# Kernel optimization log

Measured on AMD Instinct MI355X. Metric: run time of the kernel, lower is better.

The kernel has to match this reference:

```python
import jax, jax.numpy as jnp
import numpy as np

B, S, D, H, HD, FF, L = 16384, 5, 6, 2, 3, 2048, 4
EPS = 1e-5


def setup_inputs() -> dict:
    key = jax.random.key(0)
    ks = jax.random.split(key, 20)
    s = lambda fan: 1.0 / np.sqrt(fan)
    inp = {
        'x': jax.random.normal(ks[0], (B, S, D), dtype=jnp.float32),
        # per-layer stacked MHA params (in_proj split into q/k/v) and out_proj
        'Wq': jax.random.uniform(ks[1], (L, D, D), jnp.float32, -s(D), s(D)),
        'bq': jax.random.uniform(ks[2], (L, D), jnp.float32, -s(D), s(D)),
        'Wk': jax.random.uniform(ks[3], (L, D, D), jnp.float32, -s(D), s(D)),
        'bk': jax.random.uniform(ks[4], (L, D), jnp.float32, -s(D), s(D)),
        'Wv': jax.random.uniform(ks[5], (L, D, D), jnp.float32, -s(D), s(D)),
        'bv': jax.random.uniform(ks[6], (L, D), jnp.float32, -s(D), s(D)),
        'Wo': jax.random.uniform(ks[7], (L, D, D), jnp.float32, -s(D), s(D)),
        'bo': jax.random.uniform(ks[8], (L, D), jnp.float32, -s(D), s(D)),
        # FFN: linear1 D->FF, linear2 FF->D (torch Linear stores [out,in])
        'W1': jax.random.uniform(ks[9], (L, FF, D), jnp.float32, -s(D), s(D)),
        'b1': jax.random.uniform(ks[10], (L, FF), jnp.float32, -s(D), s(D)),
        'W2': jax.random.uniform(ks[11], (L, D, FF), jnp.float32, -s(FF), s(FF)),
        'b2': jax.random.uniform(ks[12], (L, D), jnp.float32, -s(FF), s(FF)),
        # layernorms
        'g1': jnp.ones((L, D), jnp.float32),
        'be1': jnp.zeros((L, D), jnp.float32),
        'g2': jnp.ones((L, D), jnp.float32),
        'be2': jnp.zeros((L, D), jnp.float32),
        # classification head Linear(30, 2)
        'Wfc': jax.random.uniform(ks[13], (2, S * D), jnp.float32, -s(S * D), s(S * D)),
        'bfc': jax.random.uniform(ks[14], (2,), jnp.float32, -s(S * D), s(S * D)),
    }
    return inp


def _layernorm(x, g, b):
    m = jnp.mean(x, axis=-1, keepdims=True)
    v = jnp.mean(jnp.square(x - m), axis=-1, keepdims=True)
    return (x - m) * jax.lax.rsqrt(v + EPS) * g + b


def _encoder_stack(x, Wq, bq, Wk, bk, Wv, bv, Wo, bo, W1, b1, W2, b2, g1, be1, g2, be2):
    scale = 1.0 / np.sqrt(HD)
    for i in range(L):  # small fixed loop over layers
        # multi-head self-attention (post-norm, eval mode: dropout = identity)
        q = (x @ Wq[i].T + bq[i]).reshape(B, S, H, HD)
        k = (x @ Wk[i].T + bk[i]).reshape(B, S, H, HD)
        v = (x @ Wv[i].T + bv[i]).reshape(B, S, H, HD)
        scores = jnp.einsum('bqhd,bkhd->bhqk', q, k) * scale
        attn = jax.nn.softmax(scores, axis=-1)
        ctx = jnp.einsum('bhqk,bkhd->bqhd', attn, v).reshape(B, S, D)
        x = _layernorm(x + ctx @ Wo[i].T + bo[i], g1[i], be1[i])
        # FFN: relu(x W1^T + b1) W2^T + b2
        h = jax.nn.relu(x @ W1[i].T + b1[i])  # [B,S,FF]
        x = _layernorm(x + h @ W2[i].T + b2[i], g2[i], be2[i])
    return x


def reference(x, Wq, bq, Wk, bk, Wv, bv, Wo, bo, W1, b1, W2, b2, g1, be1, g2, be2, Wfc, bfc):
    t = _encoder_stack(x, Wq, bq, Wk, bk, Wv, bv, Wo, bo, W1, b1, W2, b2, g1, be1, g2, be2)
    flat = t.reshape(-1, S * D)
    logits = flat @ Wfc.T + bfc
    return jax.nn.softmax(logits, axis=1)
```

## Files before the change

kernel.cpp:

```cpp
#include <hip/hip_runtime.h>
#include <math.h>

#define NL 4
#define NBATCH 16384
#define NS 5
#define ND 6
#define NH 2
#define NHD 3
#define NFF 2048
#define EPSV 1e-5f

#define ITEMS 32
#define TPB 512
#define NPAIR 64
#define ROW (NS * ND)
#define NVAL (ITEMS * ROW)

typedef __fp16 v8h __attribute__((ext_vector_type(8)));
typedef __fp16 v2h __attribute__((ext_vector_type(2)));
typedef float f32x4 __attribute__((ext_vector_type(4)));

union HU8 { uint4 u; v8h h; __fp16 f[8]; };

__device__ inline unsigned pk_u32(float a, float b) {
    union { v2h h; unsigned u; } x;
    x.h = __builtin_amdgcn_cvt_pkrtz(a, b);
    return x.u;
}
__device__ inline unsigned packh(float a, float b) {
    union { __fp16 h[2]; unsigned u; } x;
    x.h[0] = (__fp16)a; x.h[1] = (__fp16)b; return x.u;
}

__device__ __align__(16) uint4 W1A[NL * NPAIR * 64];
__device__ __align__(16) uint4 W1B[NL * NPAIR * 64];
__device__ __align__(16) uint4 W2P[NL * NPAIR * 64];

__global__ void pack_kernel(const float* __restrict__ W1,
                            const float* __restrict__ b1,
                            const float* __restrict__ W2) {
    const int TOT = NL * NPAIR * 64;
    int idx = blockIdx.x * 256 + threadIdx.x;
    if (idx >= 3 * TOT) return;
    int arr = idx / TOT, t = idx - arr * TOT;
    int lane = t & 63, p = (t >> 6) & 63, l = t >> 12;
    int r = lane & 15, g = lane >> 4;
    HU8 o; o.u = make_uint4(0u, 0u, 0u, 0u);
    if (arr < 2) {
        if (g == 0) {
            int j = (2 * p + arr) * 16 + r;
#pragma unroll
            for (int e = 0; e < ND; ++e)
                o.f[e] = (__fp16)W1[(size_t)(l * NFF + j) * ND + e];
            o.f[6] = (__fp16)b1[l * NFF + j];
            o.f[7] = (__fp16)0.f;
        }
        if (arr == 0) W1A[t] = o.u; else W1B[t] = o.u;
    } else {
        if (r < ND) {
#pragma unroll
            for (int e = 0; e < 8; ++e) {
                int j = p * 32 + ((e < 4) ? (4 * g + e) : (16 + 4 * g + e - 4));
                o.f[e] = (__fp16)W2[(size_t)(l * ND + r) * NFF + j];
            }
        }
        W2P[t] = o.u;
    }
}

__global__ __launch_bounds__(TPB, 4) void encoder_kernel(
    const float* __restrict__ xin,
    const float* __restrict__ Wq, const float* __restrict__ bq,
    const float* __restrict__ Wk, const float* __restrict__ bk,
    const float* __restrict__ Wv, const float* __restrict__ bv,
    const float* __restrict__ Wo, const float* __restrict__ bo,
    const float* __restrict__ b2,
    const float* __restrict__ g1, const float* __restrict__ be1,
    const float* __restrict__ g2, const float* __restrict__ be2,
    const float* __restrict__ Wfc, const float* __restrict__ bfc,
    float* __restrict__ out) {
    __shared__ float xs[NVAL];
    __shared__ float kvs[ITEMS * NS * 2 * ND];
    __shared__ float ybuf[4 * 2 * 5 * 64 * 4];

    const int tid = threadIdx.x;
    const int base = blockIdx.x * ITEMS;

    if (tid < NVAL / 4)
        ((float4*)xs)[tid] = ((const float4*)(xin + (size_t)base * ROW))[tid];
    __syncthreads();

    const bool act = tid < ITEMS * NS;
    const int ai = tid / NS;
    const int at = tid - ai * NS;

    const int lane = tid & 63;
    const int w = tid >> 6;
    const int jq = w & 3, ig = w >> 2;
    const int c16 = lane & 15, g = lane >> 4;

    v8h z8; z8 = (v8h)(__fp16)0.f;
    const f32x4 cz = {0.f, 0.f, 0.f, 0.f};

    for (int l = 0; l < NL; ++l) {
        const uint4* pw1a = W1A + (size_t)(l * NPAIR + jq * 16) * 64 + lane;
        const uint4* pw1b = W1B + (size_t)(l * NPAIR + jq * 16) * 64 + lane;
        const uint4* pw2  = W2P + (size_t)(l * NPAIR + jq * 16) * 64 + lane;
        uint4 wpf[2][6];
#pragma unroll
        for (int pp = 0; pp < 2; ++pp) {
            wpf[0][pp * 3 + 0] = pw1a[pp * 64];
            wpf[0][pp * 3 + 1] = pw1b[pp * 64];
            wpf[0][pp * 3 + 2] = pw2[pp * 64];
        }

        float xr[ND], qv[ND];
        if (act) {
#pragma unroll
            for (int d = 0; d < ND; ++d) xr[d] = xs[(ai * NS + at) * ND + d];
#pragma unroll
            for (int d = 0; d < ND; ++d) {
                float aq = bq[l * ND + d], ak = bk[l * ND + d], av = bv[l * ND + d];
#pragma unroll
                for (int e = 0; e < ND; ++e) {
                    aq += Wq[(l * ND + d) * ND + e] * xr[e];
                    ak += Wk[(l * ND + d) * ND + e] * xr[e];
                    av += Wv[(l * ND + d) * ND + e] * xr[e];
                }
                qv[d] = aq;
                kvs[(ai * NS + at) * 2 * ND + d] = ak;
                kvs[(ai * NS + at) * 2 * ND + ND + d] = av;
            }
        }
        __syncthreads();
        if (act) {
            const float scale = 0.57735026919f;
            float ctx[ND];
#pragma unroll
            for (int h = 0; h < NH; ++h) {
                float sc[NS];
                float mx = -1e30f;
#pragma unroll
                for (int u = 0; u < NS; ++u) {
                    float s = 0.f;
#pragma unroll
                    for (int d = 0; d < NHD; ++d)
                        s += qv[h * NHD + d] * kvs[(ai * NS + u) * 2 * ND + h * NHD + d];
                    s *= scale;
                    sc[u] = s;
                    mx = fmaxf(mx, s);
                }
                float sum = 0.f;
#pragma unroll
                for (int u = 0; u < NS; ++u) {
                    sc[u] = __expf(sc[u] - mx);
                    sum += sc[u];
                }
                float inv = 1.f / sum;
#pragma unroll
                for (int d = 0; d < NHD; ++d) {
                    float cx = 0.f;
#pragma unroll
                    for (int u = 0; u < NS; ++u)
                        cx += sc[u] * kvs[(ai * NS + u) * 2 * ND + ND + h * NHD + d];
                    ctx[h * NHD + d] = cx * inv;
                }
            }
            float yr[ND];
#pragma unroll
            for (int d = 0; d < ND; ++d) {
                float a = bo[l * ND + d];
#pragma unroll
                for (int e = 0; e < ND; ++e) a += Wo[(l * ND + d) * ND + e] * ctx[e];
                yr[d] = a + xr[d];
            }
            float m = 0.f;
#pragma unroll
            for (int d = 0; d < ND; ++d) m += yr[d];
            m *= (1.f / ND);
            float va = 0.f;
#pragma unroll
            for (int d = 0; d < ND; ++d) { float dv = yr[d] - m; va += dv * dv; }
            va *= (1.f / ND);
            float r = rsqrtf(va + EPSV);
#pragma unroll
            for (int d = 0; d < ND; ++d)
                xs[(ai * NS + at) * ND + d] =
                    (yr[d] - m) * r * g1[l * ND + d] + be1[l * ND + d];
        }
        __syncthreads();
        v8h xb[5];
#pragma unroll
        for (int mt = 0; mt < 5; ++mt) {
            HU8 u; u.u = make_uint4(0u, 0u, 0u, 0u);
            if (g == 0) {
                int row = ig * 80 + mt * 16 + c16;
                const float* xp = &xs[row * 6];
                u.u.x = pk_u32(xp[0], xp[1]);
                u.u.y = pk_u32(xp[2], xp[3]);
                u.u.z = pk_u32(xp[4], xp[5]);
                u.u.w = 0x00003c00u;
            }
            xb[mt] = u.h;
        }
        f32x4 y0 = cz, y1 = cz, y2 = cz, y3 = cz, y4 = cz;
#pragma unroll
        for (int gq = 0; gq < 8; ++gq) {
            const int cur = gq & 1, nxt = cur ^ 1;
            if (gq < 7) {
#pragma unroll
                for (int pp = 0; pp < 2; ++pp) {
                    int pofs = (gq * 2 + 2 + pp) * 64;
                    wpf[nxt][pp * 3 + 0] = pw1a[pofs];
                    wpf[nxt][pp * 3 + 1] = pw1b[pofs];
                    wpf[nxt][pp * 3 + 2] = pw2[pofs];
                }
            }
#pragma unroll
            for (int pp = 0; pp < 2; ++pp) {
                HU8 a1; a1.u = wpf[cur][pp * 3 + 0];
                HU8 b1f; b1f.u = wpf[cur][pp * 3 + 1];
                HU8 w2f; w2f.u = wpf[cur][pp * 3 + 2];
#define FFN_STEP(YREG, XB)                                                      \
                {                                                               \
                    f32x4 h0 = __builtin_amdgcn_mfma_f32_16x16x32_f16(          \
                        a1.h, (XB), cz, 0, 0, 0);                               \
                    f32x4 h1 = __builtin_amdgcn_mfma_f32_16x16x32_f16(          \
                        b1f.h, (XB), cz, 0, 0, 0);                              \
                    HU8 hb;                                                     \
                    hb.u.x = pk_u32(h0.x, h0.y);                                \
                    hb.u.y = pk_u32(h0.z, h0.w);                                \
                    hb.u.z = pk_u32(h1.x, h1.y);                                \
                    hb.u.w = pk_u32(h1.z, h1.w);                                \
                    hb.h = __builtin_elementwise_max(hb.h, z8);                 \
                    YREG = __builtin_amdgcn_mfma_f32_16x16x32_f16(              \
                        w2f.h, hb.h, YREG, 0, 0, 0);                            \
                }
                FFN_STEP(y0, xb[0])
                FFN_STEP(y1, xb[1])
                FFN_STEP(y2, xb[2])
                FFN_STEP(y3, xb[3])
                FFN_STEP(y4, xb[4])
#undef FFN_STEP
            }
        }
        {
            f32x4* yb = (f32x4*)ybuf;
            int sb = ((jq * 2 + ig) * 5) * 64 + lane;
            yb[sb + 0 * 64] = y0;
            yb[sb + 1 * 64] = y1;
            yb[sb + 2 * 64] = y2;
            yb[sb + 3 * 64] = y3;
            yb[sb + 4 * 64] = y4;
        }
        __syncthreads();
        if (act) {
            int R = ai * NS + at;
            int igR = R / 80, rm = R % 80;
            int mtR = rm / 16, cR = rm & 15;
            float yr[ND];
#pragma unroll
            for (int d = 0; d < ND; ++d) {
                int gR = d >> 2, iR = d & 3;
                float s = 0.f;
#pragma unroll
                for (int q = 0; q < 4; ++q)
                    s += ybuf[(((q * 2 + igR) * 5 + mtR) * 64 + gR * 16 + cR) * 4 + iR];
                yr[d] = xs[R * ND + d] + s + b2[l * ND + d];
            }
            float m = 0.f;
#pragma unroll
            for (int d = 0; d < ND; ++d) m += yr[d];
            m *= (1.f / ND);
            float va = 0.f;
#pragma unroll
            for (int d = 0; d < ND; ++d) { float dv = yr[d] - m; va += dv * dv; }
            va *= (1.f / ND);
            float r = rsqrtf(va + EPSV);
#pragma unroll
            for (int d = 0; d < ND; ++d)
                xs[R * ND + d] = (yr[d] - m) * r * g2[l * ND + d] + be2[l * ND + d];
        }
        __syncthreads();
    }
    if (tid < ITEMS) {
        float l0 = bfc[0], l1 = bfc[1];
#pragma unroll
        for (int v = 0; v < ROW; ++v) {
            float xv = xs[tid * ROW + v];
            l0 += Wfc[v] * xv;
            l1 += Wfc[ROW + v] * xv;
        }
        float mx = fmaxf(l0, l1);
        float e0 = __expf(l0 - mx), e1 = __expf(l1 - mx);
        float inv = 1.f / (e0 + e1);
        out[(size_t)(base + tid) * 2 + 0] = e0 * inv;
        out[(size_t)(base + tid) * 2 + 1] = e1 * inv;
    }
}

extern "C" void kernel_launch(void* const* d_in, const int* in_sizes, int n_in,
                              void* d_out, int out_size, void* d_ws, size_t ws_size,
                              hipStream_t stream) {
    (void)in_sizes; (void)n_in; (void)d_ws; (void)ws_size; (void)out_size;
    const float* x = (const float*)d_in[0];
    const float* Wq = (const float*)d_in[1];
    const float* bq = (const float*)d_in[2];
    const float* Wk = (const float*)d_in[3];
    const float* bk = (const float*)d_in[4];
    const float* Wv = (const float*)d_in[5];
    const float* bv = (const float*)d_in[6];
    const float* Wo = (const float*)d_in[7];
    const float* bo = (const float*)d_in[8];
    const float* W1 = (const float*)d_in[9];
    const float* b1 = (const float*)d_in[10];
    const float* W2 = (const float*)d_in[11];
    const float* b2 = (const float*)d_in[12];
    const float* g1 = (const float*)d_in[13];
    const float* be1 = (const float*)d_in[14];
    const float* g2 = (const float*)d_in[15];
    const float* be2 = (const float*)d_in[16];
    const float* Wfc = (const float*)d_in[17];
    const float* bfc = (const float*)d_in[18];
    float* out = (float*)d_out;

    const int npack = 3 * NL * NPAIR * 64;
    hipLaunchKernelGGL(pack_kernel, dim3((npack + 255) / 256), dim3(256), 0, stream,
                       W1, b1, W2);
    hipLaunchKernelGGL(encoder_kernel, dim3(NBATCH / ITEMS), dim3(TPB), 0, stream,
                       x, Wq, bq, Wk, bk, Wv, bv, Wo, bo, b2, g1, be1, g2, be2,
                       Wfc, bfc, out);
}
```

Baseline: 61.68 us.

## Warp-specialize encoder: MFMA FFN waves overlap attention waves across half-batches

Splits the block into four MFMA waves that run the FFN and four scalar waves that run attention, layernorm and the classifier head, pipelined over two half-batches of 16 items across 10 stages. Each stage overlaps the FFN of one half with the attention or post-FFN norm of the other half. The classifier head is fused into the final norm stage. Only the low half of lanes writes MFMA partials, and s_setprio raises MFMA wave priority. The MFMA waves now process 80 rows per stage instead of splitting by ig, so each stage does serial work on fewer waves, at the cost of more barriers.

```diff
diff --git a/kernel.cpp b/kernel.cpp
--- a/kernel.cpp
+++ b/kernel.cpp
@@ -15,6 +15,7 @@
 #define NPAIR 64
 #define ROW (NS * ND)
 #define NVAL (ITEMS * ROW)
+#define HROWS 80
 
 typedef __fp16 v8h __attribute__((ext_vector_type(8)));
 typedef __fp16 v2h __attribute__((ext_vector_type(2)));
@@ -26,10 +27,6 @@
     union { v2h h; unsigned u; } x;
     x.h = __builtin_amdgcn_cvt_pkrtz(a, b);
     return x.u;
-}
-__device__ inline unsigned packh(float a, float b) {
-    union { __fp16 h[2]; unsigned u; } x;
-    x.h[0] = (__fp16)a; x.h[1] = (__fp16)b; return x.u;
 }
 
 __device__ __align__(16) uint4 W1A[NL * NPAIR * 64];
@@ -80,222 +77,260 @@
     const float* __restrict__ Wfc, const float* __restrict__ bfc,
     float* __restrict__ out) {
     __shared__ float xs[NVAL];
-    __shared__ float kvs[ITEMS * NS * 2 * ND];
-    __shared__ float ybuf[4 * 2 * 5 * 64 * 4];
+    __shared__ float ybuf[2 * 4 * 5 * 32 * 4];
+    __shared__ float kvs[2 * 16 * NS * 12];
 
     const int tid = threadIdx.x;
     const int base = blockIdx.x * ITEMS;
 
     if (tid < NVAL / 4)
         ((float4*)xs)[tid] = ((const float4*)(xin + (size_t)base * ROW))[tid];
-    __syncthreads();
-
-    const bool act = tid < ITEMS * NS;
-    const int ai = tid / NS;
-    const int at = tid - ai * NS;
 
     const int lane = tid & 63;
     const int w = tid >> 6;
-    const int jq = w & 3, ig = w >> 2;
+    const int jq = w & 3;
     const int c16 = lane & 15, g = lane >> 4;
+    const int tid2 = tid & 255;
+    const int aiL = tid2 >> 4;
+    const int u = tid2 & 15;
 
     v8h z8; z8 = (v8h)(__fp16)0.f;
     const f32x4 cz = {0.f, 0.f, 0.f, 0.f};
 
-    for (int l = 0; l < NL; ++l) {
-        const uint4* pw1a = W1A + (size_t)(l * NPAIR + jq * 16) * 64 + lane;
-        const uint4* pw1b = W1B + (size_t)(l * NPAIR + jq * 16) * 64 + lane;
-        const uint4* pw2  = W2P + (size_t)(l * NPAIR + jq * 16) * 64 + lane;
-        uint4 wpf[2][6];
-#pragma unroll
-        for (int pp = 0; pp < 2; ++pp) {
-            wpf[0][pp * 3 + 0] = pw1a[pp * 64];
-            wpf[0][pp * 3 + 1] = pw1b[pp * 64];
-            wpf[0][pp * 3 + 2] = pw2[pp * 64];
-        }
-
-        float xr[ND], qv[ND];
-        if (act) {
-#pragma unroll
-            for (int d = 0; d < ND; ++d) xr[d] = xs[(ai * NS + at) * ND + d];
-#pragma unroll
-            for (int d = 0; d < ND; ++d) {
-                float aq = bq[l * ND + d], ak = bk[l * ND + d], av = bv[l * ND + d];
-#pragma unroll
-                for (int e = 0; e < ND; ++e) {
-                    aq += Wq[(l * ND + d) * ND + e] * xr[e];
-                    ak += Wk[(l * ND + d) * ND + e] * xr[e];
-                    av += Wv[(l * ND + d) * ND + e] * xr[e];
-                }
-                qv[d] = aq;
-                kvs[(ai * NS + at) * 2 * ND + d] = ak;
-                kvs[(ai * NS + at) * 2 * ND + ND + d] = av;
+    for (int k = 0; k <= 9; ++k) {
+        __syncthreads();
+        if (w < 4) {
+            if (k >= 1 && k <= 8) {
+                const int hf = (k - 1) & 1, lf = (k - 1) >> 1;
+                const uint4* pw1a = W1A + (size_t)(lf * NPAIR + jq * 16) * 64 + lane;
+                const uint4* pw1b = W1B + (size_t)(lf * NPAIR + jq * 16) * 64 + lane;
+                const uint4* pw2  = W2P + (size_t)(lf * NPAIR + jq * 16) * 64 + lane;
+                uint4 wpf[2][6];
+#pragma unroll
+                for (int pp = 0; pp < 2; ++pp) {
+                    wpf[0][pp * 3 + 0] = pw1a[pp * 64];
+                    wpf[0][pp * 3 + 1] = pw1b[pp * 64];
+                    wpf[0][pp * 3 + 2] = pw2[pp * 64];
+                }
+                v8h xb[5];
+#pragma unroll
+                for (int mt = 0; mt < 5; ++mt) {
+                    HU8 ux; ux.u = make_uint4(0u, 0u, 0u, 0u);
+                    if (g == 0) {
+                        int row = hf * HROWS + mt * 16 + c16;
+                        const float* xp = &xs[row * ND];
+                        ux.u.x = pk_u32(xp[0], xp[1]);
+                        ux.u.y = pk_u32(xp[2], xp[3]);
+                        ux.u.z = pk_u32(xp[4], xp[5]);
+                        ux.u.w = 0x00003c00u;
+                    }
+                    xb[mt] = ux.h;
+                }
+                f32x4 y0 = cz, y1 = cz, y2 = cz, y3 = cz, y4 = cz;
+                __builtin_amdgcn_s_setprio(1);
+#pragma unroll
+                for (int gq = 0; gq < 8; ++gq) {
+                    const int cur = gq & 1, nxt = cur ^ 1;
+                    if (gq < 7) {
+#pragma unroll
+                        for (int pp = 0; pp < 2; ++pp) {
+                            int pofs = (gq * 2 + 2 + pp) * 64;
+                            wpf[nxt][pp * 3 + 0] = pw1a[pofs];
+                            wpf[nxt][pp * 3 + 1] = pw1b[pofs];
+                            wpf[nxt][pp * 3 + 2] = pw2[pofs];
+                        }
+                    }
+#pragma unroll
+                    for (int pp = 0; pp < 2; ++pp) {
+                        HU8 a1; a1.u = wpf[cur][pp * 3 + 0];
+                        HU8 b1f; b1f.u = wpf[cur][pp * 3 + 1];
+                        HU8 w2f; w2f.u = wpf[cur][pp * 3 + 2];
+#define FFN_STEP(YREG, XB)                                                      \
+                        {                                                       \
+                            f32x4 h0 = __builtin_amdgcn_mfma_f32_16x16x32_f16(  \
+                                a1.h, (XB), cz, 0, 0, 0);                       \
+                            f32x4 h1 = __builtin_amdgcn_mfma_f32_16x16x32_f16(  \
+                                b1f.h, (XB), cz, 0, 0, 0);                      \
+                            HU8 hb;                                             \
+                            hb.u.x = pk_u32(h0.x, h0.y);                        \
+                            hb.u.y = pk_u32(h0.z, h0.w);                        \
+                            hb.u.z = pk_u32(h1.x, h1.y);                        \
+                            hb.u.w = pk_u32(h1.z, h1.w);                        \
+                            hb.h = __builtin_elementwise_max(hb.h, z8);         \
+                            YREG = __builtin_amdgcn_mfma_f32_16x16x32_f16(      \
+                                w2f.h, hb.h, YREG, 0, 0, 0);                    \
+                        }
+                        FFN_STEP(y0, xb[0])
+                        FFN_STEP(y1, xb[1])
+                        FFN_STEP(y2, xb[2])
+                        FFN_STEP(y3, xb[3])
+                        FFN_STEP(y4, xb[4])
+#undef FFN_STEP
+                    }
+                }
+                __builtin_amdgcn_s_setprio(0);
+                if (lane < 32) {
+                    f32x4* yb4 = (f32x4*)ybuf;
+                    int sb = ((hf * 4 + jq) * 5) * 32 + lane;
+                    yb4[sb + 0 * 32] = y0;
+                    yb4[sb + 1 * 32] = y1;
+                    yb4[sb + 2 * 32] = y2;
+                    yb4[sb + 3 * 32] = y3;
+                    yb4[sb + 4 * 32] = y4;
+                }
+            }
+        } else {
+            if (k <= 7) {
+                const int ha = k & 1, la = k >> 1;
+                if (u < NS) {
+                    const int ai = ha * 16 + aiL;
+                    const int R = ai * NS + u;
+                    const int hr = aiL * 5 + u;
+                    const int mtR = hr >> 4, cR = hr & 15;
+                    float xr[ND];
+                    if (la == 0) {
+#pragma unroll
+                        for (int e = 0; e < ND; ++e) xr[e] = xs[R * ND + e];
+                    } else {
+                        const int lp = la - 1;
+                        float yr[ND];
+#pragma unroll
+                        for (int d = 0; d < ND; ++d) {
+                            float s = 0.f;
+#pragma unroll
+                            for (int q = 0; q < 4; ++q)
+                                s += ybuf[(((ha * 4 + q) * 5 + mtR) * 32 +
+                                           (d >> 2) * 16 + cR) * 4 + (d & 3)];
+                            yr[d] = xs[R * ND + d] + s + b2[lp * ND + d];
+                        }
+                        float m = 0.f;
+#pragma unroll
+                        for (int d = 0; d < ND; ++d) m += yr[d];
+                        m *= (1.f / ND);
+                        float va = 0.f;
+#pragma unroll
+                        for (int d = 0; d < ND; ++d) { float dv = yr[d] - m; va += dv * dv; }
+                        va *= (1.f / ND);
+                        float r = rsqrtf(va + EPSV);
+#pragma unroll
+                        for (int d = 0; d < ND; ++d)
+                            xr[d] = (yr[d] - m) * r * g2[lp * ND + d] + be2[lp * ND + d];
+                    }
+                    float qr[ND], kr[ND], vr[ND];
+#pragma unroll
+                    for (int d = 0; d < ND; ++d) {
+                        float aq = bq[la * ND + d], ak = bk[la * ND + d], av = bv[la * ND + d];
+#pragma unroll
+                        for (int e = 0; e < ND; ++e) {
+                            aq += Wq[(la * ND + d) * ND + e] * xr[e];
+                            ak += Wk[(la * ND + d) * ND + e] * xr[e];
+                            av += Wv[(la * ND + d) * ND + e] * xr[e];
+                        }
+                        qr[d] = aq; kr[d] = ak; vr[d] = av;
+                    }
+                    const int gb = (ha * 16 + aiL) * NS;
+#pragma unroll
+                    for (int d = 0; d < ND; ++d) {
+                        kvs[(gb + u) * 12 + d] = kr[d];
+                        kvs[(gb + u) * 12 + 6 + d] = vr[d];
+                    }
+                    __builtin_amdgcn_wave_barrier();
+                    const float scale = 0.57735026919f;
+                    float cf[ND];
+#pragma unroll
+                    for (int h = 0; h < NH; ++h) {
+                        float sc[NS];
+                        float mx = -1e30f;
+#pragma unroll
+                        for (int u2 = 0; u2 < NS; ++u2) {
+                            float s = 0.f;
+#pragma unroll
+                            for (int c = 0; c < NHD; ++c)
+                                s += qr[h * NHD + c] * kvs[(gb + u2) * 12 + h * NHD + c];
+                            s *= scale;
+                            sc[u2] = s;
+                            mx = fmaxf(mx, s);
+                        }
+                        float sum = 0.f;
+#pragma unroll
+                        for (int u2 = 0; u2 < NS; ++u2) { sc[u2] = __expf(sc[u2] - mx); sum += sc[u2]; }
+                        float inv = 1.f / sum;
+#pragma unroll
+                        for (int c = 0; c < NHD; ++c) {
+                            float cx = 0.f;
+#pragma unroll
+                            for (int u2 = 0; u2 < NS; ++u2)
+                                cx += sc[u2] * kvs[(gb + u2) * 12 + 6 + h * NHD + c];
+                            cf[h * NHD + c] = cx * inv;
+                        }
+                    }
+                    float yo[ND];
+#pragma unroll
+                    for (int d = 0; d < ND; ++d) {
+                        float a = bo[la * ND + d];
+#pragma unroll
+                        for (int e = 0; e < ND; ++e) a += Wo[(la * ND + d) * ND + e] * cf[e];
+                        yo[d] = a + xr[d];
+                    }
+                    float m1 = 0.f;
+#pragma unroll
+                    for (int d = 0; d < ND; ++d) m1 += yo[d];
+                    m1 *= (1.f / ND);
+                    float v1 = 0.f;
+#pragma unroll
+                    for (int d = 0; d < ND; ++d) { float dv = yo[d] - m1; v1 += dv * dv; }
+                    v1 *= (1.f / ND);
+                    float r1 = rsqrtf(v1 + EPSV);
+#pragma unroll
+                    for (int d = 0; d < ND; ++d)
+                        xs[R * ND + d] = (yo[d] - m1) * r1 * g1[la * ND + d] + be1[la * ND + d];
+                }
+            } else {
+                const int hd = k & 1;
+                if (u < 2) {
+                    const int ai = hd * 16 + aiL;
+                    float acc = bfc[u];
+#pragma unroll
+                    for (int t = 0; t < NS; ++t) {
+                        const int R = ai * NS + t;
+                        const int hr = aiL * 5 + t;
+                        const int mtR = hr >> 4, cR = hr & 15;
+                        float yr[ND];
+#pragma unroll
+                        for (int d = 0; d < ND; ++d) {
+                            float s = 0.f;
+#pragma unroll
+                            for (int q = 0; q < 4; ++q)
+                                s += ybuf[(((hd * 4 + q) * 5 + mtR) * 32 +
+                                           (d >> 2) * 16 + cR) * 4 + (d & 3)];
+                            yr[d] = xs[R * ND + d] + s + b2[3 * ND + d];
+                        }
+                        float m = 0.f;
+#pragma unroll
+                        for (int d = 0; d < ND; ++d) m += yr[d];
+                        m *= (1.f / ND);
+                        float va = 0.f;
+#pragma unroll
+                        for (int d = 0; d < ND; ++d) { float dv = yr[d] - m; va += dv * dv; }
+                        va *= (1.f / ND);
+                        float r = rsqrtf(va + EPSV);
+#pragma unroll
+                        for (int d = 0; d < ND; ++d) {
+                            float xv = (yr[d] - m) * r * g2[3 * ND + d] + be2[3 * ND + d];
+                            acc += Wfc[u * ROW + t * ND + d] * xv;
+                        }
+                    }
+                    kvs[(hd * 16 + aiL) * 12 + u] = acc;
+                    __builtin_amdgcn_wave_barrier();
+                    float l0 = kvs[(hd * 16 + aiL) * 12 + 0];
+                    float l1 = kvs[(hd * 16 + aiL) * 12 + 1];
+                    float mxv = fmaxf(l0, l1);
+                    float e0 = __expf(l0 - mxv), e1 = __expf(l1 - mxv);
+                    float pv = (u == 0) ? (e0 / (e0 + e1)) : (e1 / (e0 + e1));
+                    out[(size_t)(base + ai) * 2 + u] = pv;
+                }
             }
         }
-        __syncthreads();
-        if (act) {
-            const float scale = 0.57735026919f;
-            float ctx[ND];
-#pragma unroll
-            for (int h = 0; h < NH; ++h) {
-                float sc[NS];
-                float mx = -1e30f;
-#pragma unroll
-                for (int u = 0; u < NS; ++u) {
-                    float s = 0.f;
-#pragma unroll
-                    for (int d = 0; d < NHD; ++d)
-                        s += qv[h * NHD + d] * kvs[(ai * NS + u) * 2 * ND + h * NHD + d];
-                    s *= scale;
-                    sc[u] = s;
-                    mx = fmaxf(mx, s);
-                }
-                float sum = 0.f;
-#pragma unroll
-                for (int u = 0; u < NS; ++u) {
-                    sc[u] = __expf(sc[u] - mx);
-                    sum += sc[u];
-                }
-                float inv = 1.f / sum;
-#pragma unroll
-                for (int d = 0; d < NHD; ++d) {
-                    float cx = 0.f;
-#pragma unroll
-                    for (int u = 0; u < NS; ++u)
-                        cx += sc[u] * kvs[(ai * NS + u) * 2 * ND + ND + h * NHD + d];
-                    ctx[h * NHD + d] = cx * inv;
-                }
-            }
-            float yr[ND];
-#pragma unroll
-            for (int d = 0; d < ND; ++d) {
-                float a = bo[l * ND + d];
-#pragma unroll
-                for (int e = 0; e < ND; ++e) a += Wo[(l * ND + d) * ND + e] * ctx[e];
-                yr[d] = a + xr[d];
-            }
-            float m = 0.f;
-#pragma unroll
-            for (int d = 0; d < ND; ++d) m += yr[d];
-            m *= (1.f / ND);
-            float va = 0.f;
-#pragma unroll
-            for (int d = 0; d < ND; ++d) { float dv = yr[d] - m; va += dv * dv; }
-            va *= (1.f / ND);
-            float r = rsqrtf(va + EPSV);
-#pragma unroll
-            for (int d = 0; d < ND; ++d)
-                xs[(ai * NS + at) * ND + d] =
-                    (yr[d] - m) * r * g1[l * ND + d] + be1[l * ND + d];
-        }
-        __syncthreads();
-        v8h xb[5];
-#pragma unroll
-        for (int mt = 0; mt < 5; ++mt) {
-            HU8 u; u.u = make_uint4(0u, 0u, 0u, 0u);
-            if (g == 0) {
-                int row = ig * 80 + mt * 16 + c16;
-                const float* xp = &xs[row * 6];
-                u.u.x = pk_u32(xp[0], xp[1]);
-                u.u.y = pk_u32(xp[2], xp[3]);
-                u.u.z = pk_u32(xp[4], xp[5]);
-                u.u.w = 0x00003c00u;
-            }
-            xb[mt] = u.h;
-        }
-        f32x4 y0 = cz, y1 = cz, y2 = cz, y3 = cz, y4 = cz;
-#pragma unroll
-        for (int gq = 0; gq < 8; ++gq) {
-            const int cur = gq & 1, nxt = cur ^ 1;
-            if (gq < 7) {
-#pragma unroll
-                for (int pp = 0; pp < 2; ++pp) {
-                    int pofs = (gq * 2 + 2 + pp) * 64;
-                    wpf[nxt][pp * 3 + 0] = pw1a[pofs];
-                    wpf[nxt][pp * 3 + 1] = pw1b[pofs];
-                    wpf[nxt][pp * 3 + 2] = pw2[pofs];
-                }
-            }
-#pragma unroll
-            for (int pp = 0; pp < 2; ++pp) {
-                HU8 a1; a1.u = wpf[cur][pp * 3 + 0];
-                HU8 b1f; b1f.u = wpf[cur][pp * 3 + 1];
-                HU8 w2f; w2f.u = wpf[cur][pp * 3 + 2];
-#define FFN_STEP(YREG, XB)                                                      \
-                {                                                               \
-                    f32x4 h0 = __builtin_amdgcn_mfma_f32_16x16x32_f16(          \
-                        a1.h, (XB), cz, 0, 0, 0);                               \
-                    f32x4 h1 = __builtin_amdgcn_mfma_f32_16x16x32_f16(          \
-                        b1f.h, (XB), cz, 0, 0, 0);                              \
-                    HU8 hb;                                                     \
-                    hb.u.x = pk_u32(h0.x, h0.y);                                \
-                    hb.u.y = pk_u32(h0.z, h0.w);                                \
-                    hb.u.z = pk_u32(h1.x, h1.y);                                \
-                    hb.u.w = pk_u32(h1.z, h1.w);                                \
-                    hb.h = __builtin_elementwise_max(hb.h, z8);                 \
-                    YREG = __builtin_amdgcn_mfma_f32_16x16x32_f16(              \
-                        w2f.h, hb.h, YREG, 0, 0, 0);                            \
-                }
-                FFN_STEP(y0, xb[0])
-                FFN_STEP(y1, xb[1])
-                FFN_STEP(y2, xb[2])
-                FFN_STEP(y3, xb[3])
-                FFN_STEP(y4, xb[4])
-#undef FFN_STEP
-            }
-        }
-        {
-            f32x4* yb = (f32x4*)ybuf;
-            int sb = ((jq * 2 + ig) * 5) * 64 + lane;
-            yb[sb + 0 * 64] = y0;
-            yb[sb + 1 * 64] = y1;
-            yb[sb + 2 * 64] = y2;
-            yb[sb + 3 * 64] = y3;
-            yb[sb + 4 * 64] = y4;
-        }
-        __syncthreads();
-        if (act) {
-            int R = ai * NS + at;
-            int igR = R / 80, rm = R % 80;
-            int mtR = rm / 16, cR = rm & 15;
-            float yr[ND];
-#pragma unroll
-            for (int d = 0; d < ND; ++d) {
-                int gR = d >> 2, iR = d & 3;
-                float s = 0.f;
-#pragma unroll
-                for (int q = 0; q < 4; ++q)
-                    s += ybuf[(((q * 2 + igR) * 5 + mtR) * 64 + gR * 16 + cR) * 4 + iR];
-                yr[d] = xs[R * ND + d] + s + b2[l * ND + d];
-            }
-            float m = 0.f;
-#pragma unroll
-            for (int d = 0; d < ND; ++d) m += yr[d];
-            m *= (1.f / ND);
-            float va = 0.f;
-#pragma unroll
-            for (int d = 0; d < ND; ++d) { float dv = yr[d] - m; va += dv * dv; }
-            va *= (1.f / ND);
-            float r = rsqrtf(va + EPSV);
-#pragma unroll
-            for (int d = 0; d < ND; ++d)
-                xs[R * ND + d] = (yr[d] - m) * r * g2[l * ND + d] + be2[l * ND + d];
-        }
-        __syncthreads();
-    }
-    if (tid < ITEMS) {
-        float l0 = bfc[0], l1 = bfc[1];
-#pragma unroll
-        for (int v = 0; v < ROW; ++v) {
-            float xv = xs[tid * ROW + v];
-            l0 += Wfc[v] * xv;
-            l1 += Wfc[ROW + v] * xv;
-        }
-        float mx = fmaxf(l0, l1);
-        float e0 = __expf(l0 - mx), e1 = __expf(l1 - mx);
-        float inv = 1.f / (e0 + e1);
-        out[(size_t)(base + tid) * 2 + 0] = e0 * inv;
-        out[(size_t)(base + tid) * 2 + 1] = e1 * inv;
     }
 }
 
```

Measured after the change: 76.27 us. 23.7% more time.

## Halve block to 16 items/256 threads, trim ybuf, raise wave priority in FFN

Applied to the files above, without the earlier changes.

Each block now processes 16 batch items with 4 waves instead of 32 items with 8 waves, so each wave covers all 80 rows in its FF quarter and the item-group split goes away. The FFN partial-sum buffer shrinks, and only the 32 lanes holding useful output rows write it. s_setprio raises wave priority around the MFMA loop. The change doubles the number of blocks and cuts LDS per block, which may improve occupancy and latency hiding. The cost is that each FF weight fragment loaded is reused across half as many items, doubling total weight traffic.

```diff
diff --git a/kernel.cpp b/kernel.cpp
--- a/kernel.cpp
+++ b/kernel.cpp
@@ -10,8 +10,8 @@
 #define NFF 2048
 #define EPSV 1e-5f
 
-#define ITEMS 32
-#define TPB 512
+#define ITEMS 16
+#define TPB 256
 #define NPAIR 64
 #define ROW (NS * ND)
 #define NVAL (ITEMS * ROW)
@@ -26,10 +26,6 @@
     union { v2h h; unsigned u; } x;
     x.h = __builtin_amdgcn_cvt_pkrtz(a, b);
     return x.u;
-}
-__device__ inline unsigned packh(float a, float b) {
-    union { __fp16 h[2]; unsigned u; } x;
-    x.h[0] = (__fp16)a; x.h[1] = (__fp16)b; return x.u;
 }
 
 __device__ __align__(16) uint4 W1A[NL * NPAIR * 64];
@@ -80,8 +76,8 @@
     const float* __restrict__ Wfc, const float* __restrict__ bfc,
     float* __restrict__ out) {
     __shared__ float xs[NVAL];
+    __shared__ float ybuf[4 * 5 * 32 * 4];
     __shared__ float kvs[ITEMS * NS * 2 * ND];
-    __shared__ float ybuf[4 * 2 * 5 * 64 * 4];
 
     const int tid = threadIdx.x;
     const int base = blockIdx.x * ITEMS;
@@ -95,8 +91,7 @@
     const int at = tid - ai * NS;
 
     const int lane = tid & 63;
-    const int w = tid >> 6;
-    const int jq = w & 3, ig = w >> 2;
+    const int jq = tid >> 6;
     const int c16 = lane & 15, g = lane >> 4;
 
     v8h z8; z8 = (v8h)(__fp16)0.f;
@@ -192,18 +187,19 @@
         v8h xb[5];
 #pragma unroll
         for (int mt = 0; mt < 5; ++mt) {
-            HU8 u; u.u = make_uint4(0u, 0u, 0u, 0u);
+            HU8 ux; ux.u = make_uint4(0u, 0u, 0u, 0u);
             if (g == 0) {
-                int row = ig * 80 + mt * 16 + c16;
-                const float* xp = &xs[row * 6];
-                u.u.x = pk_u32(xp[0], xp[1]);
-                u.u.y = pk_u32(xp[2], xp[3]);
-                u.u.z = pk_u32(xp[4], xp[5]);
-                u.u.w = 0x00003c00u;
-            }
-            xb[mt] = u.h;
+                int row = mt * 16 + c16;
+                const float* xp = &xs[row * ND];
+                ux.u.x = pk_u32(xp[0], xp[1]);
+                ux.u.y = pk_u32(xp[2], xp[3]);
+                ux.u.z = pk_u32(xp[4], xp[5]);
+                ux.u.w = 0x00003c00u;
+            }
+            xb[mt] = ux.h;
         }
         f32x4 y0 = cz, y1 = cz, y2 = cz, y3 = cz, y4 = cz;
+        __builtin_amdgcn_s_setprio(1);
 #pragma unroll
         for (int gq = 0; gq < 8; ++gq) {
             const int cur = gq & 1, nxt = cur ^ 1;
@@ -244,20 +240,20 @@
 #undef FFN_STEP
             }
         }
-        {
-            f32x4* yb = (f32x4*)ybuf;
-            int sb = ((jq * 2 + ig) * 5) * 64 + lane;
-            yb[sb + 0 * 64] = y0;
-            yb[sb + 1 * 64] = y1;
-            yb[sb + 2 * 64] = y2;
-            yb[sb + 3 * 64] = y3;
-            yb[sb + 4 * 64] = y4;
+        __builtin_amdgcn_s_setprio(0);
+        if (lane < 32) {
+            f32x4* yb4 = (f32x4*)ybuf;
+            int sb = (jq * 5) * 32 + lane;
+            yb4[sb + 0 * 32] = y0;
+            yb4[sb + 1 * 32] = y1;
+            yb4[sb + 2 * 32] = y2;
+            yb4[sb + 3 * 32] = y3;
+            yb4[sb + 4 * 32] = y4;
         }
         __syncthreads();
         if (act) {
             int R = ai * NS + at;
-            int igR = R / 80, rm = R % 80;
-            int mtR = rm / 16, cR = rm & 15;
+            int mtR = R >> 4, cR = R & 15;
             float yr[ND];
 #pragma unroll
             for (int d = 0; d < ND; ++d) {
@@ -265,7 +261,7 @@
                 float s = 0.f;
 #pragma unroll
                 for (int q = 0; q < 4; ++q)
-                    s += ybuf[(((q * 2 + igR) * 5 + mtR) * 64 + gR * 16 + cR) * 4 + iR];
+                    s += ybuf[((q * 5 + mtR) * 32 + gR * 16 + cR) * 4 + iR];
                 yr[d] = xs[R * ND + d] + s + b2[l * ND + d];
             }
             float m = 0.f;
```

New measurement: 64.40 us. +4.4%, slower.
